# Performance work log

Hardware: AMD Instinct MI355X
Metric: run time of the kernel (lower is better)

The kernel has to match this reference:

```python
import jax, jax.numpy as jnp
import numpy as np

B, S, E, H = 2, 2048, 1024, 16
D = E // H  # head dim = 64


def setup_inputs() -> dict:
    key = jax.random.key(0)
    ks = jax.random.split(key, 8)
    return {
        "query": jax.random.normal(ks[0], (B, S, E), dtype=jnp.float32),
        "key": jax.random.normal(ks[1], (B, S, E), dtype=jnp.float32),
        "value": jax.random.normal(ks[2], (B, S, E), dtype=jnp.float32),
        "qkv_weight": jax.random.normal(ks[3], (3 * E, E), dtype=jnp.float32) * 0.02,
        "qkv_bias": jax.random.normal(ks[4], (3 * E,), dtype=jnp.float32) * 0.02,
        "proj_weight": jax.random.normal(ks[5], (E, E), dtype=jnp.float32) * 0.02,
        "proj_bias": jax.random.normal(ks[6], (E,), dtype=jnp.float32) * 0.02,
        "mask": jax.random.normal(ks[7], (S, S), dtype=jnp.float32),
    }


def reference(query, key, value, qkv_weight, qkv_bias, proj_weight, proj_bias, mask):
    # Split fused QKV weight/bias into per-projection chunks ([E,E] each).
    wq, wk, wv = jnp.split(qkv_weight, 3, axis=0)
    bq, bk, bv = jnp.split(qkv_bias, 3, axis=0)

    def proj_heads(x, w, b):
        # [B,S,E] @ [E,E]^T + [E] -> [B,H,S,D]
        y = jnp.einsum("bse,fe->bsf", x, w) + b
        return y.reshape(B, S, H, D).transpose(0, 2, 1, 3)

    q = proj_heads(query, wq, bq)
    k = proj_heads(key, wk, bk)
    v = proj_heads(value, wv, bv)

    scale = 1.0 / jnp.sqrt(jnp.asarray(D, dtype=q.dtype))
    # scores: [B,H,S,S]; mask_type 0 -> additive [S,S] float mask broadcast over B,H
    scores = jnp.einsum("bhsd,bhtd->bhst", q, k) * scale + mask[None, None, :, :]
    attn = jax.nn.softmax(scores, axis=-1)
    ctx = jnp.einsum("bhst,bhtd->bhsd", attn, v)  # [B,H,S,D]
    ctx = ctx.transpose(0, 2, 1, 3).reshape(B, S, E)
    # output projection
    return jnp.einsum("bse,fe->bsf", ctx, proj_weight) + proj_bias
```

## Files before the change

### kernel.cpp

```cpp
#include <hip/hip_runtime.h>
#include <hip/hip_bf16.h>

typedef unsigned short u16;
typedef __attribute__((ext_vector_type(8))) __bf16 bf16x8;
typedef __attribute__((ext_vector_type(4))) __bf16 bf16x4;
typedef __attribute__((ext_vector_type(4))) float f32x4;

#define LOG2E 1.44269504f

#if __has_builtin(__builtin_amdgcn_exp2f)
#define EXP2F(x) __builtin_amdgcn_exp2f(x)
#else
#define EXP2F(x) __expf((x) * 0.69314718f)
#endif

#define GLL16(gptr, lptr) \
  __builtin_amdgcn_global_load_lds((__attribute__((address_space(1))) void*)(gptr), \
                                   (__attribute__((address_space(3))) void*)(lptr), 16, 0, 0)

static __device__ __forceinline__ u16 f2bf(float f) {
  union { float f; unsigned u; } v; v.f = f;
  unsigned r = (v.u + 0x7FFFu + ((v.u >> 16) & 1u)) >> 16;
  return (u16)r;
}

__global__ __launch_bounds__(256) void cvt_all(
    const float* __restrict__ q, const float* __restrict__ k, const float* __restrict__ v,
    const float* __restrict__ w1, const float* __restrict__ w2,
    u16* __restrict__ xq, u16* __restrict__ xk, u16* __restrict__ xv,
    u16* __restrict__ wq, u16* __restrict__ wp) {
  const int b = blockIdx.x;
  const float* src; u16* dst; int off;
  if (b < 4096)       { src = q;  dst = xq; off = b; }
  else if (b < 8192)  { src = k;  dst = xk; off = b - 4096; }
  else if (b < 12288) { src = v;  dst = xv; off = b - 8192; }
  else if (b < 15360) { src = w1; dst = wq; off = b - 12288; }
  else                { src = w2; dst = wp; off = b - 15360; }
  const int i = off * 256 + threadIdx.x;
  float4 vv = ((const float4*)src)[i];
  ushort4 o;
  o.x = f2bf(vv.x); o.y = f2bf(vv.y); o.z = f2bf(vv.z); o.w = f2bf(vv.w);
  ((ushort4*)dst)[i] = o;
}

__global__ __launch_bounds__(256, 2) void qkv_gemm(
    const u16* __restrict__ xq, const u16* __restrict__ xk, const u16* __restrict__ xv,
    const u16* __restrict__ wbf, const float* __restrict__ bias,
    u16* __restrict__ qout, u16* __restrict__ kout, u16* __restrict__ vtout) {
  __shared__ u16 Al[128 * 32];
  __shared__ u16 Bl[128 * 32];
  const int tid = threadIdx.x;
  const int lane = tid & 63;
  const int w = tid >> 6;
  const int wr = w >> 1, wc = w & 1;
  const int nb = blockIdx.x, mb = blockIdx.y;
  const int row0 = mb * 128;
  const int ncol0 = nb * 128;
  const int which = nb >> 3;
  const u16* A = (which == 0) ? xq : (which == 1) ? xk : xv;
  const u16* Bw = wbf + (size_t)ncol0 * 1024;

  f32x4 acc[4][4];
  f32x4 zero = {0.f, 0.f, 0.f, 0.f};
#pragma unroll
  for (int i = 0; i < 4; i++)
#pragma unroll
    for (int j = 0; j < 4; j++) acc[i][j] = zero;

  const int srow = w * 16 + (lane >> 2);
  const int scol = (lane & 3) * 8;

  for (int k0 = 0; k0 < 1024; k0 += 32) {
#pragma unroll
    for (int p = 0; p < 2; p++) {
      const u16* ga = A + (size_t)(row0 + p * 64 + srow) * 1024 + k0 + scol;
      GLL16(ga, &Al[(p * 64 + w * 16) * 32]);
      const u16* gb = Bw + (size_t)(p * 64 + srow) * 1024 + k0 + scol;
      GLL16(gb, &Bl[(p * 64 + w * 16) * 32]);
    }
    __syncthreads();
    bf16x8 af[4], bfr[4];
#pragma unroll
    for (int mi = 0; mi < 4; mi++)
      af[mi] = *(const bf16x8*)&Al[(wr * 64 + mi * 16 + (lane & 15)) * 32 + (lane >> 4) * 8];
#pragma unroll
    for (int ni = 0; ni < 4; ni++)
      bfr[ni] = *(const bf16x8*)&Bl[(wc * 64 + ni * 16 + (lane & 15)) * 32 + (lane >> 4) * 8];
#pragma unroll
    for (int mi = 0; mi < 4; mi++)
#pragma unroll
      for (int ni = 0; ni < 4; ni++)
        acc[mi][ni] = __builtin_amdgcn_mfma_f32_16x16x32_bf16(af[mi], bfr[ni], acc[mi][ni], 0, 0, 0);
    __syncthreads();
  }

#pragma unroll
  for (int mi = 0; mi < 4; mi++) {
    const int rb = row0 + wr * 64 + mi * 16 + (lane >> 4) * 4;
#pragma unroll
    for (int ni = 0; ni < 4; ni++) {
      const int c = ncol0 + wc * 64 + ni * 16 + (lane & 15);
      const float bs = bias[c];
      const float sc = (which == 0) ? (0.125f * LOG2E) : 1.0f;
      const int fm = c & 1023;
      const int h = fm >> 6, d = fm & 63;
#pragma unroll
      for (int r = 0; r < 4; r++) {
        const int rr = rb + r;
        const int b = rr >> 11, s = rr & 2047;
        const u16 val = f2bf((acc[mi][ni][r] + bs) * sc);
        if (which == 0)
          qout[(((size_t)(b * 16 + h)) * 2048 + s) * 64 + d] = val;
        else if (which == 1)
          kout[(((size_t)(b * 16 + h)) * 2048 + s) * 64 + d] = val;
        else
          vtout[(((size_t)(b * 16 + h)) * 64 + d) * 2048 + s] = val;
      }
    }
  }
}


#define STAGE_KV(KOFF, VOFF)                                        \
  *(float4*)(ldsb + (KOFF) + S0) = kr0;                             \
  *(float2*)(ldsb + (VOFF) + VS0a) = make_float2(vr0.x, vr0.y);     \
  *(float2*)(ldsb + (VOFF) + VS0b) = make_float2(vr0.z, vr0.w);

#define ATTN_TILE(PAR, MC)                                                         \
  {                                                                                \
    f32x4 s0_, s1_, s2_, s3_;                                                      \
    __builtin_amdgcn_s_setprio(1);                                                 \
    {                                                                              \
      bf16x8 a_, b_;                                                               \
      a_ = *(const bf16x8*)(ldsb + Kr0 + 0 + (PAR));                               \
      b_ = *(const bf16x8*)(ldsb + Kr1 + 0 + (PAR));                               \
      s0_ = __builtin_amdgcn_mfma_f32_16x16x32_bf16(a_, q0, MC[0], 0, 0, 0);       \
      s0_ = __builtin_amdgcn_mfma_f32_16x16x32_bf16(b_, q1, s0_, 0, 0, 0);         \
      a_ = *(const bf16x8*)(ldsb + Kr0 + 2048 + (PAR));                            \
      b_ = *(const bf16x8*)(ldsb + Kr1 + 2048 + (PAR));                            \
      s1_ = __builtin_amdgcn_mfma_f32_16x16x32_bf16(a_, q0, MC[1], 0, 0, 0);       \
      s1_ = __builtin_amdgcn_mfma_f32_16x16x32_bf16(b_, q1, s1_, 0, 0, 0);         \
      a_ = *(const bf16x8*)(ldsb + Kr0 + 4096 + (PAR));                            \
      b_ = *(const bf16x8*)(ldsb + Kr1 + 4096 + (PAR));                            \
      s2_ = __builtin_amdgcn_mfma_f32_16x16x32_bf16(a_, q0, MC[2], 0, 0, 0);       \
      s2_ = __builtin_amdgcn_mfma_f32_16x16x32_bf16(b_, q1, s2_, 0, 0, 0);         \
      a_ = *(const bf16x8*)(ldsb + Kr0 + 6144 + (PAR));                            \
      b_ = *(const bf16x8*)(ldsb + Kr1 + 6144 + (PAR));                            \
      s3_ = __builtin_amdgcn_mfma_f32_16x16x32_bf16(a_, q0, MC[3], 0, 0, 0);       \
      s3_ = __builtin_amdgcn_mfma_f32_16x16x32_bf16(b_, q1, s3_, 0, 0, 0);         \
    }                                                                              \
    __builtin_amdgcn_s_setprio(0);                                                 \
    float pm = fmaxf(fmaxf(fmaxf(fmaxf(s0_[0], s0_[1]), fmaxf(s0_[2], s0_[3])),    \
                           fmaxf(fmaxf(s1_[0], s1_[1]), fmaxf(s1_[2], s1_[3]))),   \
                     fmaxf(fmaxf(fmaxf(s2_[0], s2_[1]), fmaxf(s2_[2], s2_[3])),    \
                           fmaxf(fmaxf(s3_[0], s3_[1]), fmaxf(s3_[2], s3_[3]))));  \
                     \
    s0_[0] = EXP2F(s0_[0] - m); s0_[1] = EXP2F(s0_[1] - m);                        \
    s0_[2] = EXP2F(s0_[2] - m); s0_[3] = EXP2F(s0_[3] - m);                        \
    s1_[0] = EXP2F(s1_[0] - m); s1_[1] = EXP2F(s1_[1] - m);                        \
    s1_[2] = EXP2F(s1_[2] - m); s1_[3] = EXP2F(s1_[3] - m);                        \
    s2_[0] = EXP2F(s2_[0] - m); s2_[1] = EXP2F(s2_[1] - m);                        \
    s2_[2] = EXP2F(s2_[2] - m); s2_[3] = EXP2F(s2_[3] - m);                        \
    s3_[0] = EXP2F(s3_[0] - m); s3_[1] = EXP2F(s3_[1] - m);                        \
    s3_[2] = EXP2F(s3_[2] - m); s3_[3] = EXP2F(s3_[3] - m);                        \
    float ps = ((s0_[0] + s0_[1]) + (s0_[2] + s0_[3])) +                           \
               ((s1_[0] + s1_[1]) + (s1_[2] + s1_[3])) +                           \
               ((s2_[0] + s2_[1]) + (s2_[2] + s2_[3])) +                           \
               ((s3_[0] + s3_[1]) + (s3_[2] + s3_[3]));                            \
    pm = fmaxf(pm, __shfl_xor(pm, 16));                                            \
    pm = fmaxf(pm, __shfl_xor(pm, 32));                                            \
    if (__any(pm > m + 8.0f)) {                 \
      const float mn = fmaxf(m, pm);                                               \
      const float al = EXP2F(m - mn);                                              \
      m = mn; lsum *= al; ps *= al;                                                \
      s0_ *= al; s1_ *= al; s2_ *= al; s3_ *= al;                                  \
      ctx[0] *= al; ctx[1] *= al; ctx[2] *= al; ctx[3] *= al;                      \
    }                                                                              \
    lsum += ps;                                                                    \
           \
    bf16x8 pa0, pa1;                                                               \
    pa0[0] = (__bf16)s0_[0]; pa0[1] = (__bf16)s0_[1];                              \
    pa0[2] = (__bf16)s0_[2]; pa0[3] = (__bf16)s0_[3];                              \
    pa0[4] = (__bf16)s1_[0]; pa0[5] = (__bf16)s1_[1];                              \
    pa0[6] = (__bf16)s1_[2]; pa0[7] = (__bf16)s1_[3];                              \
    pa1[0] = (__bf16)s2_[0]; pa1[1] = (__bf16)s2_[1];                              \
    pa1[2] = (__bf16)s2_[2]; pa1[3] = (__bf16)s2_[3];                              \
    pa1[4] = (__bf16)s3_[0]; pa1[5] = (__bf16)s3_[1];                              \
    pa1[6] = (__bf16)s3_[2]; pa1[7] = (__bf16)s3_[3];                              \
    {                                                                              \
      bf16x8 v00 = *(const bf16x8*)(ldsb + Kr0 + 16384 + (PAR));                   \
      bf16x8 v01 = *(const bf16x8*)(ldsb + Kr1 + 16384 + (PAR));                   \
      bf16x8 v10 = *(const bf16x8*)(ldsb + Kr0 + 18432 + (PAR));                   \
      bf16x8 v11 = *(const bf16x8*)(ldsb + Kr1 + 18432 + (PAR));                   \
      bf16x8 v20 = *(const bf16x8*)(ldsb + Kr0 + 20480 + (PAR));                   \
      bf16x8 v21 = *(const bf16x8*)(ldsb + Kr1 + 20480 + (PAR));                   \
      bf16x8 v30 = *(const bf16x8*)(ldsb + Kr0 + 22528 + (PAR));                   \
      bf16x8 v31 = *(const bf16x8*)(ldsb + Kr1 + 22528 + (PAR));                   \
      __builtin_amdgcn_s_setprio(1);                                               \
      ctx[0] = __builtin_amdgcn_mfma_f32_16x16x32_bf16(v00, pa0, ctx[0], 0, 0, 0); \
      ctx[0] = __builtin_amdgcn_mfma_f32_16x16x32_bf16(v01, pa1, ctx[0], 0, 0, 0); \
      ctx[1] = __builtin_amdgcn_mfma_f32_16x16x32_bf16(v10, pa0, ctx[1], 0, 0, 0); \
      ctx[1] = __builtin_amdgcn_mfma_f32_16x16x32_bf16(v11, pa1, ctx[1], 0, 0, 0); \
      ctx[2] = __builtin_amdgcn_mfma_f32_16x16x32_bf16(v20, pa0, ctx[2], 0, 0, 0); \
      ctx[2] = __builtin_amdgcn_mfma_f32_16x16x32_bf16(v21, pa1, ctx[2], 0, 0, 0); \
      ctx[3] = __builtin_amdgcn_mfma_f32_16x16x32_bf16(v30, pa0, ctx[3], 0, 0, 0); \
      ctx[3] = __builtin_amdgcn_mfma_f32_16x16x32_bf16(v31, pa1, ctx[3], 0, 0, 0); \
      __builtin_amdgcn_s_setprio(0);                                               \
    }                                                                              \
  }

__global__ __launch_bounds__(512, 4) void attn_fwd(
    const u16* __restrict__ qbf, const u16* __restrict__ kbf, const u16* __restrict__ vtbf,
    const float* __restrict__ mask, u16* __restrict__ ctxout) {
  __shared__ u16 lds[16384];
  char* ldsb = (char*)lds;
  const int tid = threadIdx.x, lane = tid & 63, w = tid >> 6;
  const int qL = lane & 15, g = lane >> 4;
  const int x = (qL & 7) << 4;
  const int orig = blockIdx.x;
  const int wgid = ((orig & 7) << 6) | (orig >> 3);
  const int xx = wgid >> 6, ii = wgid & 63;
  const int bh = ((xx & 3) << 3) | (ii & 7);
  const int qt = ((xx >> 2) << 3) | (ii >> 3);
  const int qbase = qt * 128;
  const size_t hbase = (size_t)bh * 2048 * 64;
  const int qrow = qbase + w * 16 + qL;

  const int Kr0 = qL * 128 + ((g * 16) ^ x);
  const int Kr1 = qL * 128 + ((g * 16 + 64) ^ x);
  const int srow = tid >> 3;
  const int scol = (tid & 7) * 8;
  const int S0 = srow * 128 + (((tid & 7) * 16) ^ ((srow & 7) << 4));
  const int a_ = tid & 7;
  const int vW1 = ((a_ >> 2) << 6) + (((2 * a_) & 3) << 4) + (((a_ >> 1) & 1) << 3);
  const int vW2 = ((a_ >> 2) << 6) + (((2 * a_ + 1) & 3) << 4) + (((a_ >> 1) & 1) << 3);
  const int sxr = (srow & 7) << 4;
  const int VS0a = srow * 128 + (vW1 ^ sxr);
  const int VS0b = srow * 128 + (vW2 ^ sxr);

  bf16x8 q0 = *(const bf16x8*)&qbf[hbase + (size_t)qrow * 64 + g * 8];
  bf16x8 q1 = *(const bf16x8*)&qbf[hbase + (size_t)qrow * 64 + 32 + g * 8];

  float4 kr0, vr0;
  kr0 = *(const float4*)&kbf[hbase + (size_t)srow * 64 + scol];
  vr0 = *(const float4*)&vtbf[hbase + (size_t)srow * 2048 + scol];
  STAGE_KV(0, 16384)
  kr0 = *(const float4*)&kbf[hbase + (size_t)(64 + srow) * 64 + scol];
  vr0 = *(const float4*)&vtbf[hbase + (size_t)srow * 2048 + 64 + scol];

  const u16* kp = kbf + hbase + (size_t)(128 + srow) * 64 + scol;
  const u16* vp = vtbf + hbase + (size_t)srow * 2048 + 128 + scol;
  const float* mp = mask + (size_t)qrow * 2048 + g * 4;

  f32x4 mA[4], mB[4];
#pragma unroll
  for (int tb = 0; tb < 4; tb++)
    mA[tb] = (*(const f32x4*)(mp + tb * 16)) * LOG2E;

  float m = 0.f, lsum = 0.f;
  f32x4 ctx[4];
  f32x4 zero = {0.f, 0.f, 0.f, 0.f};
#pragma unroll
  for (int db = 0; db < 4; db++) ctx[db] = zero;

  __syncthreads();

  for (int i = 0; i < 16; ++i) {
    STAGE_KV(8192, 24576)
    if (i < 15) {
      kr0 = *(const float4*)kp;
      vr0 = *(const float4*)vp;
      kp += 4096; vp += 64;
    }
#pragma unroll
    for (int tb = 0; tb < 4; tb++)
      mB[tb] = (*(const f32x4*)(mp + 64 + tb * 16)) * LOG2E;
    ATTN_TILE(0, mA)
    __syncthreads();

    if (i < 15) {
      STAGE_KV(0, 16384)
      kr0 = *(const float4*)kp;
      vr0 = *(const float4*)vp;
      kp += 4096; vp += 64;
#pragma unroll
      for (int tb = 0; tb < 4; tb++)
        mA[tb] = (*(const f32x4*)(mp + 128 + tb * 16)) * LOG2E;
    }
    ATTN_TILE(8192, mB)
    mp += 128;
    __syncthreads();
  }

  lsum += __shfl_xor(lsum, 16);
  lsum += __shfl_xor(lsum, 32);
  const float inv = 1.0f / lsum;
  const int b = bh >> 4, h = bh & 15;
  u16* orow = ctxout + (size_t)(b * 2048 + qrow) * 1024 + h * 64;
#pragma unroll
  for (int db = 0; db < 4; db++) {
    bf16x4 o;
    o[0] = (__bf16)(ctx[db][0] * inv);
    o[1] = (__bf16)(ctx[db][1] * inv);
    o[2] = (__bf16)(ctx[db][2] * inv);
    o[3] = (__bf16)(ctx[db][3] * inv);
    *(bf16x4*)&orow[db * 16 + g * 4] = o;
  }
}

__global__ __launch_bounds__(256, 2) void proj_gemm(
    const u16* __restrict__ ctx, const u16* __restrict__ wbf,
    const float* __restrict__ bias, float* __restrict__ out) {
  __shared__ u16 Al[128 * 32];
  __shared__ u16 Bl[128 * 32];
  const int tid = threadIdx.x;
  const int lane = tid & 63;
  const int w = tid >> 6;
  const int wr = w >> 1, wc = w & 1;
  const int nb = blockIdx.x, mb = blockIdx.y;
  const int row0 = mb * 128;
  const int ncol0 = nb * 128;
  const u16* Bw = wbf + (size_t)ncol0 * 1024;

  f32x4 acc[4][4];
  f32x4 zero = {0.f, 0.f, 0.f, 0.f};
#pragma unroll
  for (int i = 0; i < 4; i++)
#pragma unroll
    for (int j = 0; j < 4; j++) acc[i][j] = zero;

  const int srow = w * 16 + (lane >> 2);
  const int scol = (lane & 3) * 8;

  for (int k0 = 0; k0 < 1024; k0 += 32) {
#pragma unroll
    for (int p = 0; p < 2; p++) {
      const u16* ga = ctx + (size_t)(row0 + p * 64 + srow) * 1024 + k0 + scol;
      GLL16(ga, &Al[(p * 64 + w * 16) * 32]);
      const u16* gb = Bw + (size_t)(p * 64 + srow) * 1024 + k0 + scol;
      GLL16(gb, &Bl[(p * 64 + w * 16) * 32]);
    }
    __syncthreads();
    bf16x8 af[4], bfr[4];
#pragma unroll
    for (int mi = 0; mi < 4; mi++)
      af[mi] = *(const bf16x8*)&Al[(wr * 64 + mi * 16 + (lane & 15)) * 32 + (lane >> 4) * 8];
#pragma unroll
    for (int ni = 0; ni < 4; ni++)
      bfr[ni] = *(const bf16x8*)&Bl[(wc * 64 + ni * 16 + (lane & 15)) * 32 + (lane >> 4) * 8];
#pragma unroll
    for (int mi = 0; mi < 4; mi++)
#pragma unroll
      for (int ni = 0; ni < 4; ni++)
        acc[mi][ni] = __builtin_amdgcn_mfma_f32_16x16x32_bf16(af[mi], bfr[ni], acc[mi][ni], 0, 0, 0);
    __syncthreads();
  }

#pragma unroll
  for (int mi = 0; mi < 4; mi++) {
    const int rb = row0 + wr * 64 + mi * 16 + (lane >> 4) * 4;
#pragma unroll
    for (int ni = 0; ni < 4; ni++) {
      const int c = ncol0 + wc * 64 + ni * 16 + (lane & 15);
      const float bs = bias[c];
#pragma unroll
      for (int r = 0; r < 4; r++)
        out[(size_t)(rb + r) * 1024 + c] = acc[mi][ni][r] + bs;
    }
  }
}

extern "C" void kernel_launch(void* const* d_in, const int* in_sizes, int n_in,
                              void* d_out, int out_size, void* d_ws, size_t ws_size,
                              hipStream_t stream) {
  const float* query = (const float*)d_in[0];
  const float* key   = (const float*)d_in[1];
  const float* value = (const float*)d_in[2];
  const float* qkvw  = (const float*)d_in[3];
  const float* qkvb  = (const float*)d_in[4];
  const float* projw = (const float*)d_in[5];
  const float* projb = (const float*)d_in[6];
  const float* mask  = (const float*)d_in[7];

  char* ws = (char*)d_ws;
  u16* xq    = (u16*)(ws + 0);
  u16* xk    = (u16*)(ws + 8388608);
  u16* xv    = (u16*)(ws + 16777216);
  u16* wqkv  = (u16*)(ws + 25165824);
  u16* wproj = (u16*)(ws + 31457280);
  u16* qb    = (u16*)(ws + 33554432);
  u16* kb    = (u16*)(ws + 41943040);
  u16* vt    = (u16*)(ws + 50331648);
  u16* cx    = xq;

  cvt_all<<<16384, 256, 0, stream>>>(query, key, value, qkvw, projw, xq, xk, xv, wqkv, wproj);
  qkv_gemm<<<dim3(24, 32), 256, 0, stream>>>(xq, xk, xv, wqkv, qkvb, qb, kb, vt);
  attn_fwd<<<512, 512, 0, stream>>>(qb, kb, vt, mask, cx);
  proj_gemm<<<dim3(8, 32), 256, 0, stream>>>(cx, wproj, projb, (float*)d_out);
}
```

Before: 160.6 us.

## Software-pipeline QK^T of next tile with softmax/PV of current tile using triple-buffered LDS

The attention loop now computes the QK^T scores for tile i+1 before doing softmax and PV for tile i, so MFMA work can overlap the exp and reduction work. K/V staging moves from double to triple buffering in LDS (48 KB instead of 32 KB), and the loop is unrolled by six with rotating buffer offsets. This keeps two score tiles live in registers, adding register pressure, and the larger LDS footprint may reduce occupancy at the requested 4 blocks per CU.

```diff
diff --git a/kernel.cpp b/kernel.cpp
--- a/kernel.cpp
+++ b/kernel.cpp
@@ -121,98 +121,114 @@
 }
 
 
+#define MFMA16(A, B, C) __builtin_amdgcn_mfma_f32_16x16x32_bf16(A, B, C, 0, 0, 0)
+
 #define STAGE_KV(KOFF, VOFF)                                        \
   *(float4*)(ldsb + (KOFF) + S0) = kr0;                             \
   *(float2*)(ldsb + (VOFF) + VS0a) = make_float2(vr0.x, vr0.y);     \
   *(float2*)(ldsb + (VOFF) + VS0b) = make_float2(vr0.z, vr0.w);
 
-#define ATTN_TILE(PAR, MC)                                                         \
+#define QK_TILE(KOFF, MC, SS)                                              \
+  {                                                                        \
+    bf16x8 a_, b_;                                                         \
+    __builtin_amdgcn_s_setprio(1);                                         \
+    a_ = *(const bf16x8*)(ldsb + Kr0 + 0 + (KOFF));                        \
+    b_ = *(const bf16x8*)(ldsb + Kr1 + 0 + (KOFF));                        \
+    SS[0] = MFMA16(a_, q0, MC[0]);                                         \
+    SS[0] = MFMA16(b_, q1, SS[0]);                                         \
+    a_ = *(const bf16x8*)(ldsb + Kr0 + 2048 + (KOFF));                     \
+    b_ = *(const bf16x8*)(ldsb + Kr1 + 2048 + (KOFF));                     \
+    SS[1] = MFMA16(a_, q0, MC[1]);                                         \
+    SS[1] = MFMA16(b_, q1, SS[1]);                                         \
+    a_ = *(const bf16x8*)(ldsb + Kr0 + 4096 + (KOFF));                     \
+    b_ = *(const bf16x8*)(ldsb + Kr1 + 4096 + (KOFF));                     \
+    SS[2] = MFMA16(a_, q0, MC[2]);                                         \
+    SS[2] = MFMA16(b_, q1, SS[2]);                                         \
+    a_ = *(const bf16x8*)(ldsb + Kr0 + 6144 + (KOFF));                     \
+    b_ = *(const bf16x8*)(ldsb + Kr1 + 6144 + (KOFF));                     \
+    SS[3] = MFMA16(a_, q0, MC[3]);                                         \
+    SS[3] = MFMA16(b_, q1, SS[3]);                                         \
+    __builtin_amdgcn_s_setprio(0);                                         \
+  }
+
+#define SM_PV(VOFF, SS)                                                            \
   {                                                                                \
-    f32x4 s0_, s1_, s2_, s3_;                                                      \
-    __builtin_amdgcn_s_setprio(1);                                                 \
-    {                                                                              \
-      bf16x8 a_, b_;                                                               \
-      a_ = *(const bf16x8*)(ldsb + Kr0 + 0 + (PAR));                               \
-      b_ = *(const bf16x8*)(ldsb + Kr1 + 0 + (PAR));                               \
-      s0_ = __builtin_amdgcn_mfma_f32_16x16x32_bf16(a_, q0, MC[0], 0, 0, 0);       \
-      s0_ = __builtin_amdgcn_mfma_f32_16x16x32_bf16(b_, q1, s0_, 0, 0, 0);         \
-      a_ = *(const bf16x8*)(ldsb + Kr0 + 2048 + (PAR));                            \
-      b_ = *(const bf16x8*)(ldsb + Kr1 + 2048 + (PAR));                            \
-      s1_ = __builtin_amdgcn_mfma_f32_16x16x32_bf16(a_, q0, MC[1], 0, 0, 0);       \
-      s1_ = __builtin_amdgcn_mfma_f32_16x16x32_bf16(b_, q1, s1_, 0, 0, 0);         \
-      a_ = *(const bf16x8*)(ldsb + Kr0 + 4096 + (PAR));                            \
-      b_ = *(const bf16x8*)(ldsb + Kr1 + 4096 + (PAR));                            \
-      s2_ = __builtin_amdgcn_mfma_f32_16x16x32_bf16(a_, q0, MC[2], 0, 0, 0);       \
-      s2_ = __builtin_amdgcn_mfma_f32_16x16x32_bf16(b_, q1, s2_, 0, 0, 0);         \
-      a_ = *(const bf16x8*)(ldsb + Kr0 + 6144 + (PAR));                            \
-      b_ = *(const bf16x8*)(ldsb + Kr1 + 6144 + (PAR));                            \
-      s3_ = __builtin_amdgcn_mfma_f32_16x16x32_bf16(a_, q0, MC[3], 0, 0, 0);       \
-      s3_ = __builtin_amdgcn_mfma_f32_16x16x32_bf16(b_, q1, s3_, 0, 0, 0);         \
-    }                                                                              \
-    __builtin_amdgcn_s_setprio(0);                                                 \
-    float pm = fmaxf(fmaxf(fmaxf(fmaxf(s0_[0], s0_[1]), fmaxf(s0_[2], s0_[3])),    \
-                           fmaxf(fmaxf(s1_[0], s1_[1]), fmaxf(s1_[2], s1_[3]))),   \
-                     fmaxf(fmaxf(fmaxf(s2_[0], s2_[1]), fmaxf(s2_[2], s2_[3])),    \
-                           fmaxf(fmaxf(s3_[0], s3_[1]), fmaxf(s3_[2], s3_[3]))));  \
+    float pm = fmaxf(fmaxf(fmaxf(fmaxf(SS[0][0], SS[0][1]), fmaxf(SS[0][2], SS[0][3])), \
+                           fmaxf(fmaxf(SS[1][0], SS[1][1]), fmaxf(SS[1][2], SS[1][3]))),\
+                     fmaxf(fmaxf(fmaxf(SS[2][0], SS[2][1]), fmaxf(SS[2][2], SS[2][3])), \
+                           fmaxf(fmaxf(SS[3][0], SS[3][1]), fmaxf(SS[3][2], SS[3][3]))));\
                      \
-    s0_[0] = EXP2F(s0_[0] - m); s0_[1] = EXP2F(s0_[1] - m);                        \
-    s0_[2] = EXP2F(s0_[2] - m); s0_[3] = EXP2F(s0_[3] - m);                        \
-    s1_[0] = EXP2F(s1_[0] - m); s1_[1] = EXP2F(s1_[1] - m);                        \
-    s1_[2] = EXP2F(s1_[2] - m); s1_[3] = EXP2F(s1_[3] - m);                        \
-    s2_[0] = EXP2F(s2_[0] - m); s2_[1] = EXP2F(s2_[1] - m);                        \
-    s2_[2] = EXP2F(s2_[2] - m); s2_[3] = EXP2F(s2_[3] - m);                        \
-    s3_[0] = EXP2F(s3_[0] - m); s3_[1] = EXP2F(s3_[1] - m);                        \
-    s3_[2] = EXP2F(s3_[2] - m); s3_[3] = EXP2F(s3_[3] - m);                        \
-    float ps = ((s0_[0] + s0_[1]) + (s0_[2] + s0_[3])) +                           \
-               ((s1_[0] + s1_[1]) + (s1_[2] + s1_[3])) +                           \
-               ((s2_[0] + s2_[1]) + (s2_[2] + s2_[3])) +                           \
-               ((s3_[0] + s3_[1]) + (s3_[2] + s3_[3]));                            \
+    SS[0][0] = EXP2F(SS[0][0] - m); SS[0][1] = EXP2F(SS[0][1] - m);                \
+    SS[0][2] = EXP2F(SS[0][2] - m); SS[0][3] = EXP2F(SS[0][3] - m);                \
+    SS[1][0] = EXP2F(SS[1][0] - m); SS[1][1] = EXP2F(SS[1][1] - m);                \
+    SS[1][2] = EXP2F(SS[1][2] - m); SS[1][3] = EXP2F(SS[1][3] - m);                \
+    SS[2][0] = EXP2F(SS[2][0] - m); SS[2][1] = EXP2F(SS[2][1] - m);                \
+    SS[2][2] = EXP2F(SS[2][2] - m); SS[2][3] = EXP2F(SS[2][3] - m);                \
+    SS[3][0] = EXP2F(SS[3][0] - m); SS[3][1] = EXP2F(SS[3][1] - m);                \
+    SS[3][2] = EXP2F(SS[3][2] - m); SS[3][3] = EXP2F(SS[3][3] - m);                \
+    float ps = ((SS[0][0] + SS[0][1]) + (SS[0][2] + SS[0][3])) +                   \
+               ((SS[1][0] + SS[1][1]) + (SS[1][2] + SS[1][3])) +                   \
+               ((SS[2][0] + SS[2][1]) + (SS[2][2] + SS[2][3])) +                   \
+               ((SS[3][0] + SS[3][1]) + (SS[3][2] + SS[3][3]));                    \
     pm = fmaxf(pm, __shfl_xor(pm, 16));                                            \
     pm = fmaxf(pm, __shfl_xor(pm, 32));                                            \
     if (__any(pm > m + 8.0f)) {                 \
       const float mn = fmaxf(m, pm);                                               \
       const float al = EXP2F(m - mn);                                              \
       m = mn; lsum *= al; ps *= al;                                                \
-      s0_ *= al; s1_ *= al; s2_ *= al; s3_ *= al;                                  \
+      SS[0] *= al; SS[1] *= al; SS[2] *= al; SS[3] *= al;                          \
       ctx[0] *= al; ctx[1] *= al; ctx[2] *= al; ctx[3] *= al;                      \
     }                                                                              \
     lsum += ps;                                                                    \
-           \
     bf16x8 pa0, pa1;                                                               \
-    pa0[0] = (__bf16)s0_[0]; pa0[1] = (__bf16)s0_[1];                              \
-    pa0[2] = (__bf16)s0_[2]; pa0[3] = (__bf16)s0_[3];                              \
-    pa0[4] = (__bf16)s1_[0]; pa0[5] = (__bf16)s1_[1];                              \
-    pa0[6] = (__bf16)s1_[2]; pa0[7] = (__bf16)s1_[3];                              \
-    pa1[0] = (__bf16)s2_[0]; pa1[1] = (__bf16)s2_[1];                              \
-    pa1[2] = (__bf16)s2_[2]; pa1[3] = (__bf16)s2_[3];                              \
-    pa1[4] = (__bf16)s3_[0]; pa1[5] = (__bf16)s3_[1];                              \
-    pa1[6] = (__bf16)s3_[2]; pa1[7] = (__bf16)s3_[3];                              \
+    pa0[0] = (__bf16)SS[0][0]; pa0[1] = (__bf16)SS[0][1];                          \
+    pa0[2] = (__bf16)SS[0][2]; pa0[3] = (__bf16)SS[0][3];                          \
+    pa0[4] = (__bf16)SS[1][0]; pa0[5] = (__bf16)SS[1][1];                          \
+    pa0[6] = (__bf16)SS[1][2]; pa0[7] = (__bf16)SS[1][3];                          \
+    pa1[0] = (__bf16)SS[2][0]; pa1[1] = (__bf16)SS[2][1];                          \
+    pa1[2] = (__bf16)SS[2][2]; pa1[3] = (__bf16)SS[2][3];                          \
+    pa1[4] = (__bf16)SS[3][0]; pa1[5] = (__bf16)SS[3][1];                          \
+    pa1[6] = (__bf16)SS[3][2]; pa1[7] = (__bf16)SS[3][3];                          \
     {                                                                              \
-      bf16x8 v00 = *(const bf16x8*)(ldsb + Kr0 + 16384 + (PAR));                   \
-      bf16x8 v01 = *(const bf16x8*)(ldsb + Kr1 + 16384 + (PAR));                   \
-      bf16x8 v10 = *(const bf16x8*)(ldsb + Kr0 + 18432 + (PAR));                   \
-      bf16x8 v11 = *(const bf16x8*)(ldsb + Kr1 + 18432 + (PAR));                   \
-      bf16x8 v20 = *(const bf16x8*)(ldsb + Kr0 + 20480 + (PAR));                   \
-      bf16x8 v21 = *(const bf16x8*)(ldsb + Kr1 + 20480 + (PAR));                   \
-      bf16x8 v30 = *(const bf16x8*)(ldsb + Kr0 + 22528 + (PAR));                   \
-      bf16x8 v31 = *(const bf16x8*)(ldsb + Kr1 + 22528 + (PAR));                   \
+      bf16x8 v00 = *(const bf16x8*)(ldsb + Kr0 + (VOFF) + 0);                      \
+      bf16x8 v01 = *(const bf16x8*)(ldsb + Kr1 + (VOFF) + 0);                      \
+      bf16x8 v10 = *(const bf16x8*)(ldsb + Kr0 + (VOFF) + 2048);                   \
+      bf16x8 v11 = *(const bf16x8*)(ldsb + Kr1 + (VOFF) + 2048);                   \
+      bf16x8 v20 = *(const bf16x8*)(ldsb + Kr0 + (VOFF) + 4096);                   \
+      bf16x8 v21 = *(const bf16x8*)(ldsb + Kr1 + (VOFF) + 4096);                   \
+      bf16x8 v30 = *(const bf16x8*)(ldsb + Kr0 + (VOFF) + 6144);                   \
+      bf16x8 v31 = *(const bf16x8*)(ldsb + Kr1 + (VOFF) + 6144);                   \
       __builtin_amdgcn_s_setprio(1);                                               \
-      ctx[0] = __builtin_amdgcn_mfma_f32_16x16x32_bf16(v00, pa0, ctx[0], 0, 0, 0); \
-      ctx[0] = __builtin_amdgcn_mfma_f32_16x16x32_bf16(v01, pa1, ctx[0], 0, 0, 0); \
-      ctx[1] = __builtin_amdgcn_mfma_f32_16x16x32_bf16(v10, pa0, ctx[1], 0, 0, 0); \
-      ctx[1] = __builtin_amdgcn_mfma_f32_16x16x32_bf16(v11, pa1, ctx[1], 0, 0, 0); \
-      ctx[2] = __builtin_amdgcn_mfma_f32_16x16x32_bf16(v20, pa0, ctx[2], 0, 0, 0); \
-      ctx[2] = __builtin_amdgcn_mfma_f32_16x16x32_bf16(v21, pa1, ctx[2], 0, 0, 0); \
-      ctx[3] = __builtin_amdgcn_mfma_f32_16x16x32_bf16(v30, pa0, ctx[3], 0, 0, 0); \
-      ctx[3] = __builtin_amdgcn_mfma_f32_16x16x32_bf16(v31, pa1, ctx[3], 0, 0, 0); \
+      ctx[0] = MFMA16(v00, pa0, ctx[0]); ctx[0] = MFMA16(v01, pa1, ctx[0]);        \
+      ctx[1] = MFMA16(v10, pa0, ctx[1]); ctx[1] = MFMA16(v11, pa1, ctx[1]);        \
+      ctx[2] = MFMA16(v20, pa0, ctx[2]); ctx[2] = MFMA16(v21, pa1, ctx[2]);        \
+      ctx[3] = MFMA16(v30, pa0, ctx[3]); ctx[3] = MFMA16(v31, pa1, ctx[3]);        \
       __builtin_amdgcn_s_setprio(0);                                               \
     }                                                                              \
+  }
+
+#define BODY(KQK, KSK, KSV, VPV, SN, SO, MC, MLD, DOLOAD)                  \
+  {                                                                        \
+    STAGE_KV(KSK, KSV)                                                     \
+    if (DOLOAD) {                                                          \
+      kr0 = *(const float4*)kp;                                            \
+      vr0 = *(const float4*)vp;                                            \
+      kp += 4096; vp += 64;                                                \
+    }                                                                      \
+    MLD[0] = (*(const f32x4*)(mq + 0)) * LOG2E;                            \
+    MLD[1] = (*(const f32x4*)(mq + 16)) * LOG2E;                           \
+    MLD[2] = (*(const f32x4*)(mq + 32)) * LOG2E;                           \
+    MLD[3] = (*(const f32x4*)(mq + 48)) * LOG2E;                           \
+    mq += 64;                                                              \
+    QK_TILE(KQK, MC, SN)                                                   \
+    SM_PV(VPV, SO)                                                         \
+    __syncthreads();                                                       \
   }
 
 __global__ __launch_bounds__(512, 4) void attn_fwd(
     const u16* __restrict__ qbf, const u16* __restrict__ kbf, const u16* __restrict__ vtbf,
     const float* __restrict__ mask, u16* __restrict__ ctxout) {
-  __shared__ u16 lds[16384];
+  __shared__ u16 lds[24576];
   char* ldsb = (char*)lds;
   const int tid = threadIdx.x, lane = tid & 63, w = tid >> 6;
   const int qL = lane & 15, g = lane >> 4;
@@ -244,18 +260,24 @@
   float4 kr0, vr0;
   kr0 = *(const float4*)&kbf[hbase + (size_t)srow * 64 + scol];
   vr0 = *(const float4*)&vtbf[hbase + (size_t)srow * 2048 + scol];
-  STAGE_KV(0, 16384)
+  STAGE_KV(0, 24576)
   kr0 = *(const float4*)&kbf[hbase + (size_t)(64 + srow) * 64 + scol];
   vr0 = *(const float4*)&vtbf[hbase + (size_t)srow * 2048 + 64 + scol];
-
-  const u16* kp = kbf + hbase + (size_t)(128 + srow) * 64 + scol;
-  const u16* vp = vtbf + hbase + (size_t)srow * 2048 + 128 + scol;
+  STAGE_KV(8192, 32768)
+  kr0 = *(const float4*)&kbf[hbase + (size_t)(128 + srow) * 64 + scol];
+  vr0 = *(const float4*)&vtbf[hbase + (size_t)srow * 2048 + 128 + scol];
+
+  const u16* kp = kbf + hbase + (size_t)(192 + srow) * 64 + scol;
+  const u16* vp = vtbf + hbase + (size_t)srow * 2048 + 192 + scol;
   const float* mp = mask + (size_t)qrow * 2048 + g * 4;
-
-  f32x4 mA[4], mB[4];
-#pragma unroll
-  for (int tb = 0; tb < 4; tb++)
+  const float* mq = mp + 128;
+
+  f32x4 mA[4], mB[4], sA[4], sB[4];
+#pragma unroll
+  for (int tb = 0; tb < 4; tb++) {
     mA[tb] = (*(const f32x4*)(mp + tb * 16)) * LOG2E;
+    mB[tb] = (*(const f32x4*)(mp + 64 + tb * 16)) * LOG2E;
+  }
 
   float m = 0.f, lsum = 0.f;
   f32x4 ctx[4];
@@ -264,33 +286,19 @@
   for (int db = 0; db < 4; db++) ctx[db] = zero;
 
   __syncthreads();
-
-  for (int i = 0; i < 16; ++i) {
-    STAGE_KV(8192, 24576)
-    if (i < 15) {
-      kr0 = *(const float4*)kp;
-      vr0 = *(const float4*)vp;
-      kp += 4096; vp += 64;
-    }
-#pragma unroll
-    for (int tb = 0; tb < 4; tb++)
-      mB[tb] = (*(const f32x4*)(mp + 64 + tb * 16)) * LOG2E;
-    ATTN_TILE(0, mA)
-    __syncthreads();
-
-    if (i < 15) {
-      STAGE_KV(0, 16384)
-      kr0 = *(const float4*)kp;
-      vr0 = *(const float4*)vp;
-      kp += 4096; vp += 64;
-#pragma unroll
-      for (int tb = 0; tb < 4; tb++)
-        mA[tb] = (*(const f32x4*)(mp + 128 + tb * 16)) * LOG2E;
-    }
-    ATTN_TILE(8192, mB)
-    mp += 128;
-    __syncthreads();
-  }
+  QK_TILE(0, mA, sA)
+
+  for (int j = 0; j < 5; ++j) {
+    BODY(8192,  16384, 40960, 24576, sB, sA, mB, mA, 1)
+    BODY(16384, 0,     24576, 32768, sA, sB, mA, mB, 1)
+    BODY(0,     8192,  32768, 40960, sB, sA, mB, mA, 1)
+    BODY(8192,  16384, 40960, 24576, sA, sB, mA, mB, 1)
+    BODY(16384, 0,     24576, 32768, sB, sA, mB, mA, 1)
+    BODY(0,     8192,  32768, 40960, sA, sB, mA, mB, (j < 4))
+  }
+  QK_TILE(8192, mB, sB)
+  SM_PV(24576, sA)
+  SM_PV(32768, sB)
 
   lsum += __shfl_xor(lsum, 16);
   lsum += __shfl_xor(lsum, 32);
```

Measured after the change: 174.3 us. +8.6%, slower.
